# Optimization experiments

Measured on AMD Instinct MI355X. Metric: run time of the kernel, lower is better.

## Reference

```python
import jax, jax.numpy as jnp
import numpy as np

NF, NX, GROUP_SIZE = 8192, 2048, 64
N_GROUPS = NX // GROUP_SIZE  # pad = 0 since NX % GROUP_SIZE == 0


def setup_inputs() -> dict:
    key = jax.random.key(0)
    k1, k2, k3, k4, k5 = jax.random.split(key, 5)
    x = jax.random.normal(k1, (4, 2048, NX), dtype=jnp.float32)
    packed = jax.random.randint(k2, (NF, NX // 2), 0, 256, dtype=jnp.int32)
    scales = jax.random.uniform(k3, (NF, N_GROUPS), dtype=jnp.float32)
    zeros = jax.random.randint(k4, (NF, N_GROUPS), 0, 16, dtype=jnp.int32)
    bias = jax.random.normal(k5, (NF,), dtype=jnp.float32)
    return {"x": x, "packed": packed, "scales": scales, "zeros": zeros, "bias": bias}


def _dequantize(packed, scales, zeros):
    # packed: [nf, nx//2] bytes, two int4 nibbles per byte (low nibble first)
    low = packed & 15
    high = (packed >> 4) & 15
    # interleave: q[:, 0::2] = low, q[:, 1::2] = high
    q = jnp.stack([low, high], axis=-1).reshape(NF, NX).astype(jnp.float32)
    q = q.reshape(NF, N_GROUPS, GROUP_SIZE)
    W = (q - zeros.astype(jnp.float32)[:, :, None]) * scales[:, :, None]
    return W.reshape(NF, NX)  # [nf, nx]


def reference(x, packed, scales, zeros, bias):
    W = _dequantize(packed, scales, zeros).astype(x.dtype)  # [nf, nx]
    size_out = x.shape[:-1] + (NF,)
    out = jnp.matmul(x.reshape(-1, NX), W.T) + bias  # addmm
    return out.reshape(size_out)
```

## Files before the change

kernel.cpp:

```cpp
#include <hip/hip_runtime.h>
#include <stdint.h>

#define NF 8192
#define NX 2048
#define MROWS 8192
#define NGROUPS 32
#define NT 32

typedef unsigned short u16;
typedef __bf16 bf16x8 __attribute__((ext_vector_type(8)));
typedef float f32x4 __attribute__((ext_vector_type(4)));

#define AS1 __attribute__((address_space(1)))
#define AS3 __attribute__((address_space(3)))

__device__ __forceinline__ void glds16(const void* g, void* l) {
    __builtin_amdgcn_global_load_lds((AS1 void*)(uintptr_t)g,
                                     (AS3 void*)(uintptr_t)l, 16, 0, 0);
}

__device__ __forceinline__ u16 f2bf(float f) {
    unsigned u = __float_as_uint(f);
    return (u16)((u + 0x7FFFu + ((u >> 16) & 1u)) >> 16);
}

__global__ void dequant_kernel(const int* __restrict__ packed,
                               const float* __restrict__ scales,
                               const int* __restrict__ zeros,
                               uint32_t* __restrict__ W2) {
    int tid = blockIdx.x * blockDim.x + threadIdx.x;
    int f = tid >> 10;
    int i = tid & 1023;
    int g = f * NGROUPS + (i >> 5);
    int p = packed[tid];
    float s = scales[g];
    float z = (float)zeros[g];
    float w0 = ((float)(p & 15) - z) * s;
    float w1 = ((float)((p >> 4) & 15) - z) * s;
    W2[tid] = (uint32_t)f2bf(w0) | ((uint32_t)f2bf(w1) << 16);
}

__global__ void cvt_kernel(const float4* __restrict__ x, ushort4* __restrict__ y) {
    int i = blockIdx.x * blockDim.x + threadIdx.x;
    float4 v = x[i];
    ushort4 o;
    o.x = f2bf(v.x); o.y = f2bf(v.y); o.z = f2bf(v.z); o.w = f2bf(v.w);
    y[i] = o;
}


#define BAR    __builtin_amdgcn_s_barrier()
#define LGKM8  asm volatile("s_waitcnt lgkmcnt(8)" ::: "memory")
#define LGKM0  asm volatile("s_waitcnt lgkmcnt(0)" ::: "memory")
#define VMCNT0 asm volatile("s_waitcnt vmcnt(0)" ::: "memory")
#define FENCE  __builtin_amdgcn_sched_barrier(0)

#define LD8(off) (*(const bf16x8*)(smem + (off)))

#define RD(aX, bX, BUF, SX) do { \
    _Pragma("unroll") \
    for (int i_ = 0; i_ < 4; ++i_) aX[i_] = LD8((BUF) + aOff + i_ * 2048 + (SX)); \
    _Pragma("unroll") \
    for (int j_ = 0; j_ < 4; ++j_) bX[j_] = LD8((BUF) + bOff + j_ * 2048 + (SX)); \
} while (0)

#define MM(aX, bX) do { \
    _Pragma("unroll") \
    for (int i_ = 0; i_ < 4; ++i_) \
        _Pragma("unroll") \
        for (int j_ = 0; j_ < 4; ++j_) \
            acc[i_][j_] = __builtin_amdgcn_mfma_f32_16x16x32_bf16(aX[i_], bX[j_], acc[i_][j_], 0, 0, 0); \
} while (0)

#define STAGE8(BUF, KOFF) do { \
    _Pragma("unroll") \
    for (int c_ = 0; c_ < 4; ++c_) \
        glds16(srcA + c_ * 131072 + (KOFF), smem + (BUF) + c_ * 4096 + t16); \
    _Pragma("unroll") \
    for (int c_ = 0; c_ < 4; ++c_) \
        glds16(srcB + c_ * 131072 + (KOFF), smem + (BUF) + 16384 + c_ * 4096 + t16); \
} while (0)

__global__ __launch_bounds__(256, 2)
void gemm_kernel(const u16* __restrict__ A, const u16* __restrict__ B,
                 const float* __restrict__ bias, float* __restrict__ C) {
    __shared__ __align__(16) char smem[65536];

    const int t = threadIdx.x;

    const int bid = blockIdx.x;
    const int xcd = bid & 7;
    const int local = bid >> 3;
    const int super = local >> 7;
    const int r = local & 127;
    const int by = xcd * 8 + super * 2 + (r & 1);
    const int bx = r >> 1;
    const int rowA0 = by * 128;
    const int rowB0 = bx * 128;

    const int t16 = t * 16;
    const int ulog = (t & 7) ^ ((t >> 3) & 7);
    const int koff = (ulog >> 2) * 64 + (ulog & 3) * 16;
    const char* srcA = (const char*)A + (size_t)(rowA0 + (t >> 3)) * 4096 + koff;
    const char* srcB = (const char*)B + (size_t)(rowB0 + (t >> 3)) * 4096 + koff;

    const int lane = t & 63;
    const int wv = t >> 6;
    const int wm = wv >> 1;
    const int wn = wv & 1;
    const int l15 = lane & 15;
    const int quad = lane >> 4;
    const int l7 = l15 & 7;
    const int sx0 = (quad ^ l7) << 4;
    const int sx1 = ((4 + quad) ^ l7) << 4;
    const int aOff = (wm * 64 + l15) * 128;
    const int bOff = 16384 + (wn * 64 + l15) * 128;

    f32x4 acc[4][4];
#pragma unroll
    for (int i = 0; i < 4; ++i)
#pragma unroll
        for (int j = 0; j < 4; ++j) acc[i][j] = {0.f, 0.f, 0.f, 0.f};

    bf16x8 a0[4], b0[4], a1[4], b1[4];

    STAGE8(0, 0);
    VMCNT0;

#pragma unroll 1
    for (int T = 0; T < NT; ++T) {
        const int bo = (T & 1) << 15;
        const int so = bo ^ 32768;

        FENCE; BAR; FENCE;
        if (T + 1 < NT) STAGE8(so, (T + 1) * 128);
        RD(a0, b0, bo, sx0);
        RD(a1, b1, bo, sx1);
        FENCE; LGKM8; FENCE;
        __builtin_amdgcn_s_setprio(1);
        MM(a0, b0);
        __builtin_amdgcn_s_setprio(0);
        FENCE; LGKM0; FENCE;
        __builtin_amdgcn_s_setprio(1);
        MM(a1, b1);
        __builtin_amdgcn_s_setprio(0);
        FENCE;
        VMCNT0;
    }

    const int col0 = rowB0 + wn * 64 + l15;
    const int row0 = rowA0 + wm * 64 + quad * 4;
    float bj[4];
#pragma unroll
    for (int j = 0; j < 4; ++j) bj[j] = bias[col0 + j * 16];
#pragma unroll
    for (int i = 0; i < 4; ++i) {
#pragma unroll
        for (int e = 0; e < 4; ++e) {
            float* crow = C + (size_t)(row0 + i * 16 + e) * NF;
#pragma unroll
            for (int j = 0; j < 4; ++j)
                __builtin_nontemporal_store(acc[i][j][e] + bj[j], crow + col0 + j * 16);
        }
    }
}

extern "C" void kernel_launch(void* const* d_in, const int* in_sizes, int n_in,
                              void* d_out, int out_size, void* d_ws, size_t ws_size,
                              hipStream_t stream) {
    const float* x      = (const float*)d_in[0];
    const int* packed   = (const int*)d_in[1];
    const float* scales = (const float*)d_in[2];
    const int* zeros    = (const int*)d_in[3];
    const float* bias   = (const float*)d_in[4];
    float* out = (float*)d_out;

    u16* Wq = (u16*)d_ws;
    u16* Xb = Wq + (size_t)NF * NX;

    dequant_kernel<<<(NF * (NX / 2)) / 256, 256, 0, stream>>>(packed, scales, zeros, (uint32_t*)Wq);
    cvt_kernel<<<(MROWS * NX / 4) / 256, 256, 0, stream>>>((const float4*)x, (ushort4*)Xb);

    gemm_kernel<<<dim3((MROWS / 128) * (NF / 128)), 256, 0, stream>>>(Xb, Wq, bias, out);
}
```

Measured before the change: 295.9 us.

## Enlarge GEMM tile to 256x128 with triple-buffered 32-wide K stages

Changes the GEMM block tile from 128x128 to 256x128, so each wave computes 128x64 with an 8x4 accumulator array, and halves the grid. The K loop now steps 32 elements at a time over 64 steps with a three-slot LDS ring, prefetching two stages ahead and waiting with vmcnt(6) instead of draining every iteration. The goal is more MFMA work per byte loaded and better overlap of global-to-LDS traffic with compute. The cost is double the accumulator registers, which may strain the two-blocks-per-CU launch bound, a larger 72KB LDS footprint, and a new swizzle pattern.

```diff
diff --git a/kernel.cpp b/kernel.cpp
--- a/kernel.cpp
+++ b/kernel.cpp
@@ -5,7 +5,7 @@
 #define NX 2048
 #define MROWS 8192
 #define NGROUPS 32
-#define NT 32
+#define NSTEP 64
 
 typedef unsigned short u16;
 typedef __bf16 bf16x8 __attribute__((ext_vector_type(8)));
@@ -50,41 +50,28 @@
 
 
 #define BAR    __builtin_amdgcn_s_barrier()
-#define LGKM8  asm volatile("s_waitcnt lgkmcnt(8)" ::: "memory")
 #define LGKM0  asm volatile("s_waitcnt lgkmcnt(0)" ::: "memory")
+#define VMCNT6 asm volatile("s_waitcnt vmcnt(6)" ::: "memory")
 #define VMCNT0 asm volatile("s_waitcnt vmcnt(0)" ::: "memory")
 #define FENCE  __builtin_amdgcn_sched_barrier(0)
 
 #define LD8(off) (*(const bf16x8*)(smem + (off)))
 
-#define RD(aX, bX, BUF, SX) do { \
-    _Pragma("unroll") \
-    for (int i_ = 0; i_ < 4; ++i_) aX[i_] = LD8((BUF) + aOff + i_ * 2048 + (SX)); \
-    _Pragma("unroll") \
-    for (int j_ = 0; j_ < 4; ++j_) bX[j_] = LD8((BUF) + bOff + j_ * 2048 + (SX)); \
-} while (0)
-
-#define MM(aX, bX) do { \
-    _Pragma("unroll") \
-    for (int i_ = 0; i_ < 4; ++i_) \
-        _Pragma("unroll") \
-        for (int j_ = 0; j_ < 4; ++j_) \
-            acc[i_][j_] = __builtin_amdgcn_mfma_f32_16x16x32_bf16(aX[i_], bX[j_], acc[i_][j_], 0, 0, 0); \
-} while (0)
-
-#define STAGE8(BUF, KOFF) do { \
-    _Pragma("unroll") \
-    for (int c_ = 0; c_ < 4; ++c_) \
-        glds16(srcA + c_ * 131072 + (KOFF), smem + (BUF) + c_ * 4096 + t16); \
-    _Pragma("unroll") \
-    for (int c_ = 0; c_ < 4; ++c_) \
-        glds16(srcB + c_ * 131072 + (KOFF), smem + (BUF) + 16384 + c_ * 4096 + t16); \
+#define STAGE6(REG, S) do { \
+    const char* _sa = srcA + (size_t)(S) * 64; \
+    const char* _sb = srcB + (size_t)(S) * 64; \
+    glds16(_sa,          smem + (REG) + t16); \
+    glds16(_sa + 262144, smem + (REG) + 4096  + t16); \
+    glds16(_sa + 524288, smem + (REG) + 8192  + t16); \
+    glds16(_sa + 786432, smem + (REG) + 12288 + t16); \
+    glds16(_sb,          smem + (REG) + 16384 + t16); \
+    glds16(_sb + 262144, smem + (REG) + 20480 + t16); \
 } while (0)
 
 __global__ __launch_bounds__(256, 2)
 void gemm_kernel(const u16* __restrict__ A, const u16* __restrict__ B,
                  const float* __restrict__ bias, float* __restrict__ C) {
-    __shared__ __align__(16) char smem[65536];
+    __shared__ __align__(16) char smem[73728];
 
     const int t = threadIdx.x;
 
@@ -93,16 +80,15 @@
     const int local = bid >> 3;
     const int super = local >> 7;
     const int r = local & 127;
-    const int by = xcd * 8 + super * 2 + (r & 1);
+    const int by = xcd * 4 + super * 2 + (r & 1);
     const int bx = r >> 1;
-    const int rowA0 = by * 128;
+    const int rowA0 = by * 256;
     const int rowB0 = bx * 128;
 
     const int t16 = t * 16;
-    const int ulog = (t & 7) ^ ((t >> 3) & 7);
-    const int koff = (ulog >> 2) * 64 + (ulog & 3) * 16;
-    const char* srcA = (const char*)A + (size_t)(rowA0 + (t >> 3)) * 4096 + koff;
-    const char* srcB = (const char*)B + (size_t)(rowB0 + (t >> 3)) * 4096 + koff;
+    const int kslot = (t & 3) ^ ((t >> 3) & 3);
+    const char* srcA = (const char*)A + (size_t)(rowA0 + (t >> 2)) * 4096 + kslot * 16;
+    const char* srcB = (const char*)B + (size_t)(rowB0 + (t >> 2)) * 4096 + kslot * 16;
 
     const int lane = t & 63;
     const int wv = t >> 6;
@@ -110,51 +96,54 @@
     const int wn = wv & 1;
     const int l15 = lane & 15;
     const int quad = lane >> 4;
-    const int l7 = l15 & 7;
-    const int sx0 = (quad ^ l7) << 4;
-    const int sx1 = ((4 + quad) ^ l7) << 4;
-    const int aOff = (wm * 64 + l15) * 128;
-    const int bOff = 16384 + (wn * 64 + l15) * 128;
+    const int uX = ((((l15 >> 1) & 3) ^ quad)) << 4;
+    const int aOff = (wm * 128 + l15) * 64 + uX;
+    const int bOff = 16384 + (wn * 64 + l15) * 64 + uX;
 
-    f32x4 acc[4][4];
+    f32x4 acc[8][4];
 #pragma unroll
-    for (int i = 0; i < 4; ++i)
+    for (int i = 0; i < 8; ++i)
 #pragma unroll
         for (int j = 0; j < 4; ++j) acc[i][j] = {0.f, 0.f, 0.f, 0.f};
 
-    bf16x8 a0[4], b0[4], a1[4], b1[4];
+    bf16x8 a[8], b[4];
 
-    STAGE8(0, 0);
-    VMCNT0;
+    STAGE6(0,     0);
+    STAGE6(24576, 1);
+    VMCNT6;
+
+    int regC = 0, regN = 24576, regT = 49152;
 
 #pragma unroll 1
-    for (int T = 0; T < NT; ++T) {
-        const int bo = (T & 1) << 15;
-        const int so = bo ^ 32768;
-
+    for (int s = 0; s < NSTEP; ++s) {
         FENCE; BAR; FENCE;
-        if (T + 1 < NT) STAGE8(so, (T + 1) * 128);
-        RD(a0, b0, bo, sx0);
-        RD(a1, b1, bo, sx1);
-        FENCE; LGKM8; FENCE;
-        __builtin_amdgcn_s_setprio(1);
-        MM(a0, b0);
-        __builtin_amdgcn_s_setprio(0);
+#pragma unroll
+        for (int i = 0; i < 8; ++i) a[i] = LD8(regC + aOff + i * 1024);
+#pragma unroll
+        for (int j = 0; j < 4; ++j) b[j] = LD8(regC + bOff + j * 1024);
+        if (s + 2 < NSTEP) STAGE6(regT, s + 2);
         FENCE; LGKM0; FENCE;
         __builtin_amdgcn_s_setprio(1);
-        MM(a1, b1);
+#pragma unroll
+        for (int i = 0; i < 8; ++i)
+#pragma unroll
+            for (int j = 0; j < 4; ++j)
+                acc[i][j] = __builtin_amdgcn_mfma_f32_16x16x32_bf16(a[i], b[j], acc[i][j], 0, 0, 0);
         __builtin_amdgcn_s_setprio(0);
         FENCE;
-        VMCNT0;
+        if (s + 2 < NSTEP) VMCNT6;
+        else if (s + 1 < NSTEP) VMCNT0;
+
+        const int tmp = regC; regC = regN; regN = regT; regT = tmp;
     }
 
     const int col0 = rowB0 + wn * 64 + l15;
-    const int row0 = rowA0 + wm * 64 + quad * 4;
+    const int row0 = rowA0 + wm * 128 + quad * 4;
     float bj[4];
 #pragma unroll
     for (int j = 0; j < 4; ++j) bj[j] = bias[col0 + j * 16];
 #pragma unroll
-    for (int i = 0; i < 4; ++i) {
+    for (int i = 0; i < 8; ++i) {
 #pragma unroll
         for (int e = 0; e < 4; ++e) {
             float* crow = C + (size_t)(row0 + i * 16 + e) * NF;
@@ -181,5 +170,5 @@
     dequant_kernel<<<(NF * (NX / 2)) / 256, 256, 0, stream>>>(packed, scales, zeros, (uint32_t*)Wq);
     cvt_kernel<<<(MROWS * NX / 4) / 256, 256, 0, stream>>>((const float4*)x, (ushort4*)Xb);
 
-    gemm_kernel<<<dim3((MROWS / 128) * (NF / 128)), 256, 0, stream>>>(Xb, Wq, bias, out);
+    gemm_kernel<<<dim3((MROWS / 256) * (NF / 128)), 256, 0, stream>>>(Xb, Wq, bias, out);
 }
```

New measurement: 306.3 us. 3.5% more time.

## Pre-swizzle activations into MFMA fragment layout and load A directly to registers

Applied to the files above, without the earlier changes.

The conversion kernel now writes bf16 activations in a 16x32 fragment-major layout matching the MFMA A operand. The GEMM then reads A straight from global memory into registers, double-buffered across tiles, and stages only B through LDS. This halves LDS use and LDS traffic per tile and may allow more overlap. In exchange each wave issues its own global loads for A, with no sharing through LDS between the two N-waves, and the wait counts are tuned by hand.

```diff
diff --git a/kernel.cpp b/kernel.cpp
--- a/kernel.cpp
+++ b/kernel.cpp
@@ -40,51 +40,85 @@
     W2[tid] = (uint32_t)f2bf(w0) | ((uint32_t)f2bf(w1) << 16);
 }
 
-__global__ void cvt_kernel(const float4* __restrict__ x, ushort4* __restrict__ y) {
-    int i = blockIdx.x * blockDim.x + threadIdx.x;
-    float4 v = x[i];
-    ushort4 o;
-    o.x = f2bf(v.x); o.y = f2bf(v.y); o.z = f2bf(v.z); o.w = f2bf(v.w);
-    y[i] = o;
-}
-
-
-#define BAR    __builtin_amdgcn_s_barrier()
-#define LGKM8  asm volatile("s_waitcnt lgkmcnt(8)" ::: "memory")
-#define LGKM0  asm volatile("s_waitcnt lgkmcnt(0)" ::: "memory")
-#define VMCNT0 asm volatile("s_waitcnt vmcnt(0)" ::: "memory")
-#define FENCE  __builtin_amdgcn_sched_barrier(0)
+__global__ void cvt_kernel(const float* __restrict__ x, u16* __restrict__ y) {
+    const int tid = blockIdx.x * blockDim.x + threadIdx.x;
+    const int wid = tid >> 6;
+    const int lane = tid & 63;
+    const int l15 = lane & 15;
+    const int quad = lane >> 4;
+    const int m = (wid >> 6) * 16 + l15;
+    const int k = (wid & 63) * 32 + quad * 8;
+    const float4* src = (const float4*)(x + (size_t)m * NX + k);
+    float4 v0 = src[0], v1 = src[1];
+    ushort4 lo, hi;
+    lo.x = f2bf(v0.x); lo.y = f2bf(v0.y); lo.z = f2bf(v0.z); lo.w = f2bf(v0.w);
+    hi.x = f2bf(v1.x); hi.y = f2bf(v1.y); hi.z = f2bf(v1.z); hi.w = f2bf(v1.w);
+    ushort4* dst = (ushort4*)((char*)y + (size_t)wid * 1024 + lane * 16);
+    dst[0] = lo; dst[1] = hi;
+}
+
+
+#define BAR     __builtin_amdgcn_s_barrier()
+#define LGKM4   asm volatile("s_waitcnt lgkmcnt(4)" ::: "memory")
+#define LGKM0   asm volatile("s_waitcnt lgkmcnt(0)" ::: "memory")
+#define VMCNT12 asm volatile("s_waitcnt vmcnt(12)" ::: "memory")
+#define VMCNT8  asm volatile("s_waitcnt vmcnt(8)" ::: "memory")
+#define VMCNT0  asm volatile("s_waitcnt vmcnt(0)" ::: "memory")
+#define FENCE   __builtin_amdgcn_sched_barrier(0)
 
 #define LD8(off) (*(const bf16x8*)(smem + (off)))
 
-#define RD(aX, bX, BUF, SX) do { \
-    _Pragma("unroll") \
-    for (int i_ = 0; i_ < 4; ++i_) aX[i_] = LD8((BUF) + aOff + i_ * 2048 + (SX)); \
-    _Pragma("unroll") \
-    for (int j_ = 0; j_ < 4; ++j_) bX[j_] = LD8((BUF) + bOff + j_ * 2048 + (SX)); \
+#define STAGEB(BUF, T_) do { \
+    const char* _sb = srcB + (size_t)(T_) * 128; \
+    glds16(_sb,          smem + (BUF) + t16); \
+    glds16(_sb + 131072, smem + (BUF) + 4096  + t16); \
+    glds16(_sb + 262144, smem + (BUF) + 8192  + t16); \
+    glds16(_sb + 393216, smem + (BUF) + 12288 + t16); \
 } while (0)
 
-#define MM(aX, bX) do { \
+#define TILE(T_, AC, AN) do { \
+    const int bo = ((T_) & 1) << 14; \
+    const int so = bo ^ 16384; \
+    FENCE; BAR; FENCE; \
+    _Pragma("unroll") \
+    for (int j_ = 0; j_ < 4; ++j_) b0[j_] = LD8(bo + bOff + j_ * 2048 + sx0); \
+    _Pragma("unroll") \
+    for (int j_ = 0; j_ < 4; ++j_) b1[j_] = LD8(bo + bOff + j_ * 2048 + sx1); \
+    FENCE; \
+    if ((T_) + 1 < NT) { \
+        STAGEB(so, (T_) + 1); \
+        _Pragma("unroll") \
+        for (int i_ = 0; i_ < 8; ++i_) \
+            AN[i_] = *(const bf16x8*)(aBase + (i_ >> 1) * 65536 + \
+                                      ((T_) + 1) * 2048 + (i_ & 1) * 1024); \
+    } \
+    FENCE; LGKM4; \
+    if ((T_) + 1 < NT) { VMCNT12; } else { VMCNT0; } \
+    FENCE; \
+    __builtin_amdgcn_s_setprio(1); \
     _Pragma("unroll") \
     for (int i_ = 0; i_ < 4; ++i_) \
         _Pragma("unroll") \
         for (int j_ = 0; j_ < 4; ++j_) \
-            acc[i_][j_] = __builtin_amdgcn_mfma_f32_16x16x32_bf16(aX[i_], bX[j_], acc[i_][j_], 0, 0, 0); \
+            acc[i_][j_] = __builtin_amdgcn_mfma_f32_16x16x32_bf16(AC[2 * i_], b0[j_], acc[i_][j_], 0, 0, 0); \
+    __builtin_amdgcn_s_setprio(0); \
+    FENCE; LGKM0; FENCE; \
+    __builtin_amdgcn_s_setprio(1); \
+    _Pragma("unroll") \
+    for (int i_ = 0; i_ < 4; ++i_) \
+        _Pragma("unroll") \
+        for (int j_ = 0; j_ < 4; ++j_) \
+            acc[i_][j_] = __builtin_amdgcn_mfma_f32_16x16x32_bf16(AC[2 * i_ + 1], b1[j_], acc[i_][j_], 0, 0, 0); \
+    __builtin_amdgcn_s_setprio(0); \
+    FENCE; \
+    if ((T_) + 1 < NT) VMCNT8; \
 } while (0)
 
-#define STAGE8(BUF, KOFF) do { \
-    _Pragma("unroll") \
-    for (int c_ = 0; c_ < 4; ++c_) \
-        glds16(srcA + c_ * 131072 + (KOFF), smem + (BUF) + c_ * 4096 + t16); \
-    _Pragma("unroll") \
-    for (int c_ = 0; c_ < 4; ++c_) \
-        glds16(srcB + c_ * 131072 + (KOFF), smem + (BUF) + 16384 + c_ * 4096 + t16); \
-} while (0)
-
 __global__ __launch_bounds__(256, 2)
-void gemm_kernel(const u16* __restrict__ A, const u16* __restrict__ B,
+void gemm_kernel(const u16* __restrict__ A ,
+                 const u16* __restrict__ B ,
                  const float* __restrict__ bias, float* __restrict__ C) {
-    __shared__ __align__(16) char smem[65536];
+    __shared__ __align__(16) char smem[32768];
 
     const int t = threadIdx.x;
 
@@ -100,9 +134,8 @@
 
     const int t16 = t * 16;
     const int ulog = (t & 7) ^ ((t >> 3) & 7);
-    const int koff = (ulog >> 2) * 64 + (ulog & 3) * 16;
-    const char* srcA = (const char*)A + (size_t)(rowA0 + (t >> 3)) * 4096 + koff;
-    const char* srcB = (const char*)B + (size_t)(rowB0 + (t >> 3)) * 4096 + koff;
+    const int koffB = (ulog >> 2) * 64 + (ulog & 3) * 16;
+    const char* srcB = (const char*)B + (size_t)(rowB0 + (t >> 3)) * 4096 + koffB;
 
     const int lane = t & 63;
     const int wv = t >> 6;
@@ -113,8 +146,9 @@
     const int l7 = l15 & 7;
     const int sx0 = (quad ^ l7) << 4;
     const int sx1 = ((4 + quad) ^ l7) << 4;
-    const int aOff = (wm * 64 + l15) * 128;
-    const int bOff = 16384 + (wn * 64 + l15) * 128;
+    const int bOff = (wn * 64 + l15) * 128;
+
+    const char* aBase = (const char*)A + ((size_t)(by * 8 + wm * 4) << 16) + lane * 16;
 
     f32x4 acc[4][4];
 #pragma unroll
@@ -122,30 +156,18 @@
 #pragma unroll
         for (int j = 0; j < 4; ++j) acc[i][j] = {0.f, 0.f, 0.f, 0.f};
 
-    bf16x8 a0[4], b0[4], a1[4], b1[4];
-
-    STAGE8(0, 0);
-    VMCNT0;
+    bf16x8 aA[8], aB_[8], b0[4], b1[4];
+
+    STAGEB(0, 0);
+#pragma unroll
+    for (int i = 0; i < 8; ++i)
+        aA[i] = *(const bf16x8*)(aBase + (i >> 1) * 65536 + (i & 1) * 1024);
+    VMCNT8;
 
 #pragma unroll 1
-    for (int T = 0; T < NT; ++T) {
-        const int bo = (T & 1) << 15;
-        const int so = bo ^ 32768;
-
-        FENCE; BAR; FENCE;
-        if (T + 1 < NT) STAGE8(so, (T + 1) * 128);
-        RD(a0, b0, bo, sx0);
-        RD(a1, b1, bo, sx1);
-        FENCE; LGKM8; FENCE;
-        __builtin_amdgcn_s_setprio(1);
-        MM(a0, b0);
-        __builtin_amdgcn_s_setprio(0);
-        FENCE; LGKM0; FENCE;
-        __builtin_amdgcn_s_setprio(1);
-        MM(a1, b1);
-        __builtin_amdgcn_s_setprio(0);
-        FENCE;
-        VMCNT0;
+    for (int T = 0; T < NT; T += 2) {
+        TILE(T,     aA,  aB_);
+        TILE(T + 1, aB_, aA);
     }
 
     const int col0 = rowB0 + wn * 64 + l15;
@@ -179,7 +201,7 @@
     u16* Xb = Wq + (size_t)NF * NX;
 
     dequant_kernel<<<(NF * (NX / 2)) / 256, 256, 0, stream>>>(packed, scales, zeros, (uint32_t*)Wq);
-    cvt_kernel<<<(MROWS * NX / 4) / 256, 256, 0, stream>>>((const float4*)x, (ushort4*)Xb);
+    cvt_kernel<<<(MROWS / 16) * (NX / 32) * 64 / 256, 256, 0, stream>>>(x, Xb);
 
     gemm_kernel<<<dim3((MROWS / 128) * (NF / 128)), 256, 0, stream>>>(Xb, Wq, bias, out);
 }
```

New measurement: 345.1 us. +16.6%, slower.
